# Performance work log

Hardware: AMD Instinct MI355X
Metric: run time of the kernel (lower is better)

Reference implementation:

```python
import jax, jax.numpy as jnp
import numpy as np

N_LAYERS = 2
H = 16                      # num_heads
ARW = (1.0, 1.0)            # att_residual_weight
MCB = (0.0, 1.0)            # mask_clip_balancer
LN_EPS = 1e-5


def _ln(x, g, b):
    mu = jnp.mean(x, axis=-1, keepdims=True)
    var = jnp.mean(jnp.square(x - mu), axis=-1, keepdims=True)
    return (x - mu) * jax.lax.rsqrt(var + LN_EPS) * g + b


def _quick_gelu(u):
    return u * jax.nn.sigmoid(1.702 * u)


def setup_inputs() -> dict:
    key = jax.random.key(0)
    ks = jax.random.split(key, 8)
    L, B, C = 577, 8, 1024
    d_ff = 4 * C
    inp = {
        'x': jax.random.normal(ks[0], (L, B, C), jnp.float32),
        'att_bias': jax.random.normal(ks[1], (N_LAYERS, B * H, L, L), jnp.float32),
        'ln1_g': jnp.ones((N_LAYERS, C), jnp.float32),
        'ln1_b': jnp.zeros((N_LAYERS, C), jnp.float32),
        'in_w': 0.02 * jax.random.normal(ks[2], (N_LAYERS, 3 * C, C), jnp.float32),
        'in_b': jnp.zeros((N_LAYERS, 3 * C), jnp.float32),
        'out_w': 0.02 * jax.random.normal(ks[3], (N_LAYERS, C, C), jnp.float32),
        'out_b': jnp.zeros((N_LAYERS, C), jnp.float32),
        'ln2_g': jnp.ones((N_LAYERS, C), jnp.float32),
        'ln2_b': jnp.zeros((N_LAYERS, C), jnp.float32),
        'fc1_w': 0.02 * jax.random.normal(ks[4], (N_LAYERS, d_ff, C), jnp.float32),
        'fc1_b': jnp.zeros((N_LAYERS, d_ff), jnp.float32),
        'fc2_w': 0.02 * jax.random.normal(ks[5], (N_LAYERS, C, d_ff), jnp.float32),
        'fc2_b': jnp.zeros((N_LAYERS, C), jnp.float32),
    }
    return inp


def reference(x, att_bias, ln1_g, ln1_b, in_w, in_b, out_w, out_b,
              ln2_g, ln2_b, fc1_w, fc1_b, fc2_w, fc2_b):
    L, B, C = x.shape
    d = C // H
    scale = d ** -0.5  # custom_att_factor is None
    for i in range(N_LAYERS):
        # --- custom CSA attention ---
        h = _ln(x, ln1_g[i], ln1_b[i])                              # [L,B,C]
        qkv = jnp.einsum('lbc,fc->lbf', h, in_w[i]) + in_b[i]       # [L,B,3C]
        q, k, v = jnp.split(qkv, 3, axis=-1)
        to_heads = lambda t: t.reshape(L, B, H, d).transpose(1, 2, 0, 3)  # [B,H,L,d]
        q, k, v = to_heads(q), to_heads(k), to_heads(v)
        bias = att_bias[i].reshape(B, H, L, L)
        q_attn = bias + scale * jnp.einsum('bhld,bhmd->bhlm', q, q)
        k_attn = bias + scale * jnp.einsum('bhld,bhmd->bhlm', k, k)
        attn = jax.nn.softmax(q_attn, axis=-1) + jax.nn.softmax(k_attn, axis=-1)
        attn = attn * 0.5                                           # norm_att=True
        attn = jnp.mean(attn, axis=1, keepdims=True)                # avg_att=True -> [B,1,L,L]
        out = jnp.matmul(attn, v)                                   # broadcast over H -> [B,H,L,d]
        out = MCB[0] * v + MCB[1] * out
        out = out.transpose(2, 0, 1, 3).reshape(L, B, C)
        out = jnp.einsum('lbc,oc->lbo', out, out_w[i]) + out_b[i]
        x = ARW[0] * x + ARW[1] * out
        # --- MLP residual ---
        h2 = _ln(x, ln2_g[i], ln2_b[i])
        u = _quick_gelu(jnp.einsum('lbc,fc->lbf', h2, fc1_w[i]) + fc1_b[i])
        x = x + jnp.einsum('lbf,cf->lbc', u, fc2_w[i]) + fc2_b[i]
    return x
```

## Files before the change

### kernel.cpp

```cpp
#include <hip/hip_runtime.h>

typedef float f32x4 __attribute__((ext_vector_type(4)));
typedef __bf16 bf16x8 __attribute__((ext_vector_type(8)));

#define L_SEQ 577
#define BB 8
#define CC 1024
#define HH 16
#define ROWS (L_SEQ*BB)

static __device__ __forceinline__ ushort f2b(float f) {
  unsigned u = __float_as_uint(f);
  u += 0x7fffu + ((u >> 16) & 1u);
  return (ushort)(u >> 16);
}

static __device__ __forceinline__ void gld16(const void* g, void* l) {
  __builtin_amdgcn_global_load_lds((const __attribute__((address_space(1))) void*)g,
                                   (__attribute__((address_space(3))) void*)l, 16, 0, 0);
}

__global__ void cvt_kernel(const float* __restrict__ src, ushort* __restrict__ dst, int n4) {
  int i = blockIdx.x * blockDim.x + threadIdx.x;
  if (i < n4) {
    float4 v = *(const float4*)(src + (size_t)i * 4);
    ushort4 o;
    o.x = f2b(v.x); o.y = f2b(v.y); o.z = f2b(v.z); o.w = f2b(v.w);
    *(ushort4*)(dst + (size_t)i * 4) = o;
  }
}

__global__ __launch_bounds__(256)
void ln_kernel(const float* __restrict__ x, const float* __restrict__ g,
               const float* __restrict__ be, ushort* __restrict__ out)
{
  const int row = blockIdx.x;
  const int t = threadIdx.x;
  const float* xr = x + (size_t)row * CC;
  float4 v = *(const float4*)(xr + t * 4);
  float s  = v.x + v.y + v.z + v.w;
  float s2 = v.x*v.x + v.y*v.y + v.z*v.z + v.w*v.w;
  #pragma unroll
  for (int sd = 1; sd < 64; sd <<= 1) { s += __shfl_xor(s, sd, 64); s2 += __shfl_xor(s2, sd, 64); }
  __shared__ float ps[4], ps2[4];
  const int w = t >> 6;
  if ((t & 63) == 0) { ps[w] = s; ps2[w] = s2; }
  __syncthreads();
  s  = ps[0] + ps[1] + ps[2] + ps[3];
  s2 = ps2[0] + ps2[1] + ps2[2] + ps2[3];
  const float mean = s * (1.f / 1024.f);
  const float var  = s2 * (1.f / 1024.f) - mean * mean;
  const float rstd = rsqrtf(var + 1e-5f);
  float4 gv = *(const float4*)(g + t * 4);
  float4 bv = *(const float4*)(be + t * 4);
  ushort4 o;
  o.x = f2b((v.x - mean) * rstd * gv.x + bv.x);
  o.y = f2b((v.y - mean) * rstd * gv.y + bv.y);
  o.z = f2b((v.z - mean) * rstd * gv.z + bv.z);
  o.w = f2b((v.w - mean) * rstd * gv.w + bv.w);
  *(ushort4*)(out + (size_t)row * CC + t * 4) = o;
}

__global__ __launch_bounds__(256)
void vt_kernel(const ushort* __restrict__ qkv, ushort* __restrict__ vt)
{
  __shared__ ushort tile[32][33];
  const int lt = blockIdx.x * 32;
  const int nt = blockIdx.y * 32;
  const int b  = blockIdx.z;
  const int tx = threadIdx.x & 31;
  const int ty = threadIdx.x >> 5;
  #pragma unroll
  for (int p = 0; p < 4; ++p) {
    int l = lt + ty + p * 8;
    ushort v = 0;
    if (l < L_SEQ) v = qkv[((size_t)l * BB + b) * 3072 + 2048 + nt + tx];
    tile[ty + p * 8][tx] = v;
  }
  __syncthreads();
  #pragma unroll
  for (int p = 0; p < 4; ++p) {
    int n = nt + ty + p * 8;
    int l = lt + tx;
    vt[((size_t)b * 1024 + n) * 608 + l] = tile[tx][ty + p * 8];
  }
}

__global__ __launch_bounds__(256, 2)
void attn_kernel(const ushort* __restrict__ qkv,
                 const float* __restrict__ bias,
                 float* __restrict__ attnf)
{
  __shared__ float S[2][16][612];
  const int t = threadIdx.x;
  const int lane = t & 63;
  const int w = t >> 6;
  const int rb = blockIdx.x;
  const int b  = blockIdx.y;
  const int hg = blockIdx.z;
  const int r0 = rb * 16;
  float acc[37];
  #pragma unroll
  for (int k = 0; k < 37; ++k) acc[k] = 0.f;

  const int fr = lane & 15;
  const int kc = (lane >> 4) * 8;
  const int arow = min(r0 + fr, L_SEQ - 1);
  const size_t abase = ((size_t)arow * BB + b) * 3072;

  for (int hh = 0; hh < 4; ++hh) {
    const int h = hg * 4 + hh;
    const int qoff = h * 64;
    const int koff = CC + h * 64;
    bf16x8 aq0 = *(const bf16x8*)(qkv + abase + qoff + kc);
    bf16x8 aq1 = *(const bf16x8*)(qkv + abase + qoff + 32 + kc);
    bf16x8 ak0 = *(const bf16x8*)(qkv + abase + koff + kc);
    bf16x8 ak1 = *(const bf16x8*)(qkv + abase + koff + 32 + kc);
    for (int nt = w; nt < 37; nt += 4) {
      const int col = nt * 16 + fr;
      const int ncl = min(col, L_SEQ - 1);
      const size_t brow = ((size_t)ncl * BB + b) * 3072;
      bf16x8 bq0 = *(const bf16x8*)(qkv + brow + qoff + kc);
      bf16x8 bq1 = *(const bf16x8*)(qkv + brow + qoff + 32 + kc);
      bf16x8 bk0 = *(const bf16x8*)(qkv + brow + koff + kc);
      bf16x8 bk1 = *(const bf16x8*)(qkv + brow + koff + 32 + kc);
      f32x4 dq = {0.f, 0.f, 0.f, 0.f};
      f32x4 dk = {0.f, 0.f, 0.f, 0.f};
      dq = __builtin_amdgcn_mfma_f32_16x16x32_bf16(aq0, bq0, dq, 0, 0, 0);
      dq = __builtin_amdgcn_mfma_f32_16x16x32_bf16(aq1, bq1, dq, 0, 0, 0);
      dk = __builtin_amdgcn_mfma_f32_16x16x32_bf16(ak0, bk0, dk, 0, 0, 0);
      dk = __builtin_amdgcn_mfma_f32_16x16x32_bf16(ak1, bk1, dk, 0, 0, 0);
      const bool cvalid = (col < L_SEQ);
      #pragma unroll
      for (int r = 0; r < 4; ++r) {
        int row = (lane >> 4) * 4 + r;
        int l = min(r0 + row, L_SEQ - 1);
        float bs = bias[(((size_t)(b * HH + h)) * L_SEQ + l) * L_SEQ + min(col, L_SEQ - 1)];
        S[0][row][col] = cvalid ? (bs + 0.125f * dq[r]) : -1e30f;
        S[1][row][col] = cvalid ? (bs + 0.125f * dk[r]) : -1e30f;
      }
    }
    __syncthreads();
    const int rr = t >> 4;
    const int j0 = t & 15;
    #pragma unroll
    for (int v = 0; v < 2; ++v) {
      float mx = -1e30f;
      #pragma unroll
      for (int k = 0; k < 37; ++k) mx = fmaxf(mx, S[v][rr][j0 + 16 * k]);
      #pragma unroll
      for (int sd = 1; sd < 16; sd <<= 1) mx = fmaxf(mx, __shfl_xor(mx, sd, 16));
      float e[37]; float sm = 0.f;
      #pragma unroll
      for (int k = 0; k < 37; ++k) { e[k] = __expf(S[v][rr][j0 + 16 * k] - mx); sm += e[k]; }
      #pragma unroll
      for (int sd = 1; sd < 16; sd <<= 1) sm += __shfl_xor(sm, sd, 16);
      float inv = 0.03125f / sm;
      #pragma unroll
      for (int k = 0; k < 37; ++k) acc[k] += e[k] * inv;
    }
    __syncthreads();
  }
  const int rr = t >> 4;
  const int j0 = t & 15;
  const int l = r0 + rr;
  if (l < L_SEQ) {
    float* dst = attnf + (size_t)b * 608 * 608 + (size_t)l * 608;
    #pragma unroll
    for (int k = 0; k < 37; ++k)
      if (j0 + 16 * k < L_SEQ) atomicAdd(dst + j0 + 16 * k, acc[k]);
  }
}

template<int EPI>
__global__ __launch_bounds__(256, 2)
void gemm_bt(const ushort* __restrict__ A, int lda, int Arows, long aStride,
             const ushort* __restrict__ B, int ldb, long bStride,
             int M, int N, int K, int kSplit,
             const float* __restrict__ bias,
             float* __restrict__ xio,
             ushort* __restrict__ outb, int ldo)
{
  __shared__ __align__(16) ushort As[128 * 32];
  __shared__ __align__(16) ushort Bs[128 * 32];
  const int t = threadIdx.x;
  const int lane = t & 63;
  const int w = t >> 6;
  const int bm = blockIdx.x, bn = blockIdx.y, bz = blockIdx.z;
  int k0 = 0, k1 = K;
  const ushort* Ab = A;
  const ushort* Bb = B;
  if (kSplit > 1) {
    const int kc0 = K / kSplit;
    k0 = bz * kc0; k1 = k0 + kc0;
  } else {
    Ab += (long)bz * aStride;
    Bb += (long)bz * bStride;
  }
  const int srow = t >> 2;
  const int sc = (t & 3) * 8;
  const int wr = (w >> 1) * 64;
  const int wc = (w & 1) * 64;
  const int am1 = Arows - 1;
  f32x4 acc[4][4] = {};

  const int r0a = bm * 128 + srow;
  const int r0b = bn * 128 + srow;
  for (int kt = k0; kt < k1; kt += 32) {
    __syncthreads();
    gld16(Ab + (size_t)min(r0a, am1) * lda + kt + sc, (void*)(As + t * 8));
    gld16(Ab + (size_t)min(r0a + 64, am1) * lda + kt + sc, (void*)(As + 2048 + t * 8));
    gld16(Bb + (size_t)r0b * ldb + kt + sc, (void*)(Bs + t * 8));
    gld16(Bb + (size_t)(r0b + 64) * ldb + kt + sc, (void*)(Bs + 2048 + t * 8));
    asm volatile("s_waitcnt vmcnt(0)" ::: "memory");
    __syncthreads();
    bf16x8 av[4], bv[4];
    const int fr = lane & 15;
    const int kc = (lane >> 4) * 8;
    #pragma unroll
    for (int m = 0; m < 4; ++m) av[m] = *(const bf16x8*)(As + (wr + m * 16 + fr) * 32 + kc);
    #pragma unroll
    for (int n = 0; n < 4; ++n) bv[n] = *(const bf16x8*)(Bs + (wc + n * 16 + fr) * 32 + kc);
    #pragma unroll
    for (int m = 0; m < 4; ++m)
      #pragma unroll
      for (int n = 0; n < 4; ++n)
        acc[m][n] = __builtin_amdgcn_mfma_f32_16x16x32_bf16(av[m], bv[n], acc[m][n], 0, 0, 0);
  }
  const int rbase = wr + (lane >> 4) * 4;
  const int cbase = wc + (lane & 15);
  #pragma unroll
  for (int n = 0; n < 4; ++n) {
    const int gn = bn * 128 + cbase + n * 16;
    const float bval = (EPI == 3) ? 0.f : ((k0 == 0) ? bias[gn] : 0.f);
    #pragma unroll
    for (int m = 0; m < 4; ++m) {
      f32x4 d = acc[m][n];
      #pragma unroll
      for (int r = 0; r < 4; ++r) {
        const int gm = bm * 128 + rbase + m * 16 + r;
        if (gm < M) {
          if (EPI == 0) {
            outb[(size_t)gm * ldo + gn] = f2b(d[r] + bval);
          } else if (EPI == 1) {
            float v0 = d[r] + bval;
            outb[(size_t)gm * ldo + gn] = f2b(v0 / (1.f + __expf(-1.702f * v0)));
          } else if (EPI == 2) {
            atomicAdd(xio + (size_t)gm * ldo + gn, d[r] + bval);
          } else {
            outb[((size_t)gm * 8 + bz) * ldo + gn] = f2b(d[r]);
          }
        }
      }
    }
  }
}

extern "C" void kernel_launch(void* const* d_in, const int* in_sizes, int n_in,
                              void* d_out, int out_size, void* d_ws, size_t ws_size,
                              hipStream_t stream)
{
  (void)in_sizes; (void)n_in; (void)out_size; (void)ws_size;
  const float* x_in  = (const float*)d_in[0];
  const float* attb  = (const float*)d_in[1];
  const float* ln1_g = (const float*)d_in[2];
  const float* ln1_b = (const float*)d_in[3];
  const float* in_w  = (const float*)d_in[4];
  const float* in_b  = (const float*)d_in[5];
  const float* out_w = (const float*)d_in[6];
  const float* out_b = (const float*)d_in[7];
  const float* ln2_g = (const float*)d_in[8];
  const float* ln2_b = (const float*)d_in[9];
  const float* fc1_w = (const float*)d_in[10];
  const float* fc1_b = (const float*)d_in[11];
  const float* fc2_w = (const float*)d_in[12];
  const float* fc2_b = (const float*)d_in[13];
  float* x = (float*)d_out;

  char* ws = (char*)d_ws;
  size_t off = 0;
  auto alloc = [&](size_t bytes) -> void* {
    void* p = ws + off; off += (bytes + 255) & ~(size_t)255; return p;
  };
  ushort* wIn   = (ushort*)alloc(2ull * 3072 * 1024 * 2);
  ushort* wOut  = (ushort*)alloc(2ull * 1024 * 1024 * 2);
  ushort* wF1   = (ushort*)alloc(2ull * 4096 * 1024 * 2);
  ushort* wF2   = (ushort*)alloc(2ull * 4096 * 1024 * 2);
  ushort* hbuf  = (ushort*)alloc((size_t)ROWS * 1024 * 2);
  ushort* qkv   = (ushort*)alloc((size_t)ROWS * 3072 * 2);
  ushort* vt    = (ushort*)alloc((size_t)8 * 1024 * 608 * 2);
  ushort* attn  = (ushort*)alloc((size_t)8 * 608 * 608 * 2);
  float*  attnf = (float*)alloc((size_t)8 * 608 * 608 * 4);
  ushort* outlb = (ushort*)alloc((size_t)ROWS * 1024 * 2);
  ushort* ubuf  = qkv;

  cvt_kernel<<<2 * 3072 * 1024 / 4 / 256, 256, 0, stream>>>(in_w,  wIn,  2 * 3072 * 1024 / 4);
  cvt_kernel<<<2 * 1024 * 1024 / 4 / 256, 256, 0, stream>>>(out_w, wOut, 2 * 1024 * 1024 / 4);
  cvt_kernel<<<2 * 4096 * 1024 / 4 / 256, 256, 0, stream>>>(fc1_w, wF1,  2 * 4096 * 1024 / 4);
  cvt_kernel<<<2 * 4096 * 1024 / 4 / 256, 256, 0, stream>>>(fc2_w, wF2,  2 * 4096 * 1024 / 4);
  hipMemcpyAsync(x, x_in, (size_t)ROWS * 1024 * 4, hipMemcpyDeviceToDevice, stream);

  for (int i = 0; i < 2; ++i) {
    ln_kernel<<<ROWS, 256, 0, stream>>>(x, ln1_g + i * 1024, ln1_b + i * 1024, hbuf);
    gemm_bt<0><<<dim3(37, 24, 1), 256, 0, stream>>>(hbuf, 1024, ROWS, 0,
        wIn + (size_t)i * 3072 * 1024, 1024, 0,
        ROWS, 3072, 1024, 1, in_b + i * 3072, nullptr, qkv, 3072);
    hipMemsetAsync(attnf, 0, (size_t)8 * 608 * 608 * 4, stream);
    attn_kernel<<<dim3(37, 8, 4), 256, 0, stream>>>(qkv, attb + (size_t)i * 128 * 577 * 577, attnf);
    vt_kernel<<<dim3(19, 32, 8), 256, 0, stream>>>(qkv, vt);
    cvt_kernel<<<8 * 608 * 608 / 4 / 256, 256, 0, stream>>>(attnf, attn, 8 * 608 * 608 / 4);
    gemm_bt<3><<<dim3(5, 8, 8), 256, 0, stream>>>(attn, 608, 577, (long)608 * 608,
        vt, 608, (long)1024 * 608,
        577, 1024, 608, 1, nullptr, nullptr, outlb, 1024);
    gemm_bt<2><<<dim3(37, 8, 2), 256, 0, stream>>>(outlb, 1024, ROWS, 0,
        wOut + (size_t)i * 1024 * 1024, 1024, 0,
        ROWS, 1024, 1024, 2, out_b + i * 1024, x, nullptr, 1024);
    ln_kernel<<<ROWS, 256, 0, stream>>>(x, ln2_g + i * 1024, ln2_b + i * 1024, hbuf);
    gemm_bt<1><<<dim3(37, 32, 1), 256, 0, stream>>>(hbuf, 1024, ROWS, 0,
        wF1 + (size_t)i * 4096 * 1024, 1024, 0,
        ROWS, 4096, 1024, 1, fc1_b + i * 4096, nullptr, ubuf, 4096);
    gemm_bt<2><<<dim3(37, 8, 4), 256, 0, stream>>>(ubuf, 4096, ROWS, 0,
        wF2 + (size_t)i * 4096 * 1024, 4096, 0,
        ROWS, 1024, 4096, 4, fc2_b + i * 1024, x, nullptr, 1024);
  }
}
```

Before: 1.146 ms.

## Add 256x256 pipelined GEMM with split-K partials reduced in fused LN-residual kernel

Replaces the 128x128 single-buffered GEMM for the QKV, out-proj, FC1 and FC2 projections with a 512-thread 256x256 tile kernel. The new kernel double-buffers 64-wide K tiles in a swizzled LDS layout and interleaves MFMA quadrants with async global-to-LDS loads, using barriers and setprio. Split-K outputs are no longer atomically added into x. They are written as fp32 partials and summed, together with the bias and residual, inside a new kernel that also computes the next LayerNorm, which removes the separate LN launches and the initial memcpy. The cost is 128KB of LDS per block at occupancy 1, fewer blocks (tile quantization on 4616 rows), and extra partial-buffer traffic.

New measurement: 1.912 ms. +66.9%, slower.

```diff
diff --git a/kernel.cpp b/kernel.cpp
--- a/kernel.cpp
+++ b/kernel.cpp
@@ -30,35 +30,49 @@
   }
 }
 
+template<int NP, bool DOLN>
 __global__ __launch_bounds__(256)
-void ln_kernel(const float* __restrict__ x, const float* __restrict__ g,
-               const float* __restrict__ be, ushort* __restrict__ out)
+void ln_resid_kernel(const float* __restrict__ xsrc, const float* __restrict__ parts,
+                     const float* __restrict__ cbias,
+                     const float* __restrict__ g, const float* __restrict__ be,
+                     float* __restrict__ xdst, ushort* __restrict__ hout)
 {
   const int row = blockIdx.x;
   const int t = threadIdx.x;
-  const float* xr = x + (size_t)row * CC;
-  float4 v = *(const float4*)(xr + t * 4);
-  float s  = v.x + v.y + v.z + v.w;
-  float s2 = v.x*v.x + v.y*v.y + v.z*v.z + v.w*v.w;
-  #pragma unroll
-  for (int sd = 1; sd < 64; sd <<= 1) { s += __shfl_xor(s, sd, 64); s2 += __shfl_xor(s2, sd, 64); }
-  __shared__ float ps[4], ps2[4];
-  const int w = t >> 6;
-  if ((t & 63) == 0) { ps[w] = s; ps2[w] = s2; }
-  __syncthreads();
-  s  = ps[0] + ps[1] + ps[2] + ps[3];
-  s2 = ps2[0] + ps2[1] + ps2[2] + ps2[3];
-  const float mean = s * (1.f / 1024.f);
-  const float var  = s2 * (1.f / 1024.f) - mean * mean;
-  const float rstd = rsqrtf(var + 1e-5f);
-  float4 gv = *(const float4*)(g + t * 4);
-  float4 bv = *(const float4*)(be + t * 4);
-  ushort4 o;
-  o.x = f2b((v.x - mean) * rstd * gv.x + bv.x);
-  o.y = f2b((v.y - mean) * rstd * gv.y + bv.y);
-  o.z = f2b((v.z - mean) * rstd * gv.z + bv.z);
-  o.w = f2b((v.w - mean) * rstd * gv.w + bv.w);
-  *(ushort4*)(out + (size_t)row * CC + t * 4) = o;
+  float4 v = *(const float4*)(xsrc + (size_t)row * CC + t * 4);
+  if (NP > 0) {
+    float4 c4 = *(const float4*)(cbias + t * 4);
+    v.x += c4.x; v.y += c4.y; v.z += c4.z; v.w += c4.w;
+    #pragma unroll
+    for (int p = 0; p < NP; ++p) {
+      float4 pv = *(const float4*)(parts + ((size_t)p * ROWS + row) * CC + t * 4);
+      v.x += pv.x; v.y += pv.y; v.z += pv.z; v.w += pv.w;
+    }
+  }
+  *(float4*)(xdst + (size_t)row * CC + t * 4) = v;
+  if (DOLN) {
+    float s  = v.x + v.y + v.z + v.w;
+    float s2 = v.x*v.x + v.y*v.y + v.z*v.z + v.w*v.w;
+    #pragma unroll
+    for (int sd = 1; sd < 64; sd <<= 1) { s += __shfl_xor(s, sd, 64); s2 += __shfl_xor(s2, sd, 64); }
+    __shared__ float ps[4], ps2[4];
+    const int w = t >> 6;
+    if ((t & 63) == 0) { ps[w] = s; ps2[w] = s2; }
+    __syncthreads();
+    s  = ps[0] + ps[1] + ps[2] + ps[3];
+    s2 = ps2[0] + ps2[1] + ps2[2] + ps2[3];
+    const float mean = s * (1.f / 1024.f);
+    const float var  = s2 * (1.f / 1024.f) - mean * mean;
+    const float rstd = rsqrtf(var + 1e-5f);
+    float4 gv = *(const float4*)(g + t * 4);
+    float4 bv = *(const float4*)(be + t * 4);
+    ushort4 o;
+    o.x = f2b((v.x - mean) * rstd * gv.x + bv.x);
+    o.y = f2b((v.y - mean) * rstd * gv.y + bv.y);
+    o.z = f2b((v.z - mean) * rstd * gv.z + bv.z);
+    o.w = f2b((v.w - mean) * rstd * gv.w + bv.w);
+    *(ushort4*)(hout + (size_t)row * CC + t * 4) = o;
+  }
 }
 
 __global__ __launch_bounds__(256)
@@ -172,13 +186,10 @@
   }
 }
 
-template<int EPI>
 __global__ __launch_bounds__(256, 2)
-void gemm_bt(const ushort* __restrict__ A, int lda, int Arows, long aStride,
+void av_gemm(const ushort* __restrict__ A, int lda, int Arows, long aStride,
              const ushort* __restrict__ B, int ldb, long bStride,
-             int M, int N, int K, int kSplit,
-             const float* __restrict__ bias,
-             float* __restrict__ xio,
+             int M, int K,
              ushort* __restrict__ outb, int ldo)
 {
   __shared__ __align__(16) ushort As[128 * 32];
@@ -187,16 +198,8 @@
   const int lane = t & 63;
   const int w = t >> 6;
   const int bm = blockIdx.x, bn = blockIdx.y, bz = blockIdx.z;
-  int k0 = 0, k1 = K;
-  const ushort* Ab = A;
-  const ushort* Bb = B;
-  if (kSplit > 1) {
-    const int kc0 = K / kSplit;
-    k0 = bz * kc0; k1 = k0 + kc0;
-  } else {
-    Ab += (long)bz * aStride;
-    Bb += (long)bz * bStride;
-  }
+  const ushort* Ab = A + (long)bz * aStride;
+  const ushort* Bb = B + (long)bz * bStride;
   const int srow = t >> 2;
   const int sc = (t & 3) * 8;
   const int wr = (w >> 1) * 64;
@@ -206,7 +209,7 @@
 
   const int r0a = bm * 128 + srow;
   const int r0b = bn * 128 + srow;
-  for (int kt = k0; kt < k1; kt += 32) {
+  for (int kt = 0; kt < K; kt += 32) {
     __syncthreads();
     gld16(Ab + (size_t)min(r0a, am1) * lda + kt + sc, (void*)(As + t * 8));
     gld16(Ab + (size_t)min(r0a + 64, am1) * lda + kt + sc, (void*)(As + 2048 + t * 8));
@@ -232,23 +235,149 @@
   #pragma unroll
   for (int n = 0; n < 4; ++n) {
     const int gn = bn * 128 + cbase + n * 16;
-    const float bval = (EPI == 3) ? 0.f : ((k0 == 0) ? bias[gn] : 0.f);
     #pragma unroll
     for (int m = 0; m < 4; ++m) {
       f32x4 d = acc[m][n];
       #pragma unroll
       for (int r = 0; r < 4; ++r) {
         const int gm = bm * 128 + rbase + m * 16 + r;
+        if (gm < M) outb[((size_t)gm * 8 + bz) * ldo + gn] = f2b(d[r]);
+      }
+    }
+  }
+}
+
+#define MFQ(MH, NH) \
+  _Pragma("unroll") \
+  for (int ks = 0; ks < 2; ++ks) \
+    _Pragma("unroll") \
+    for (int m = 0; m < 4; ++m) \
+      _Pragma("unroll") \
+      for (int n = 0; n < 2; ++n) \
+        acc[(MH)*4+m][(NH)*2+n] = __builtin_amdgcn_mfma_f32_16x16x32_bf16( \
+            (MH) ? Ahi[ks][m] : Alo[ks][m], (NH) ? Bhi[ks][n] : Blo[ks][n], \
+            acc[(MH)*4+m][(NH)*2+n], 0, 0, 0);
+
+#define KTILE(BOFS, KT2, MORE, DRAIN) do { \
+  _Pragma("unroll") for (int ks = 0; ks < 2; ++ks) { \
+    _Pragma("unroll") for (int m = 0; m < 4; ++m) Alo[ks][m] = rdA(BOFS, 0, ks, m); \
+    _Pragma("unroll") for (int n = 0; n < 2; ++n) Blo[ks][n] = rdB(BOFS, 0, ks, n); \
+  } \
+  asm volatile("s_waitcnt lgkmcnt(8)" ::: "memory"); \
+  __builtin_amdgcn_sched_barrier(0); \
+  __builtin_amdgcn_s_barrier(); \
+  asm volatile("s_waitcnt lgkmcnt(0)" ::: "memory"); \
+  __builtin_amdgcn_sched_barrier(0); \
+  __builtin_amdgcn_s_setprio(1); MFQ(0,0) __builtin_amdgcn_s_setprio(0); \
+  __builtin_amdgcn_s_barrier(); \
+  _Pragma("unroll") for (int ks = 0; ks < 2; ++ks) { \
+    _Pragma("unroll") for (int m = 0; m < 4; ++m) Ahi[ks][m] = rdA(BOFS, 1, ks, m); \
+    _Pragma("unroll") for (int n = 0; n < 2; ++n) Bhi[ks][n] = rdB(BOFS, 1, ks, n); \
+  } \
+  asm volatile("s_waitcnt lgkmcnt(8)" ::: "memory"); \
+  __builtin_amdgcn_sched_barrier(0); \
+  __builtin_amdgcn_s_barrier(); \
+  asm volatile("s_waitcnt lgkmcnt(0)" ::: "memory"); \
+  __builtin_amdgcn_sched_barrier(0); \
+  __builtin_amdgcn_s_setprio(1); MFQ(1,1) __builtin_amdgcn_s_setprio(0); \
+  __builtin_amdgcn_s_barrier(); \
+  if (MORE) { stageA(KT2, BOFS, 0); stageA(KT2, BOFS, 1); } \
+  __builtin_amdgcn_s_barrier(); \
+  __builtin_amdgcn_s_setprio(1); MFQ(0,1) __builtin_amdgcn_s_setprio(0); \
+  __builtin_amdgcn_s_barrier(); \
+  if (MORE) { stageB(KT2, BOFS, 0); stageB(KT2, BOFS, 1); } \
+  __builtin_amdgcn_s_barrier(); \
+  __builtin_amdgcn_s_setprio(1); MFQ(1,0) __builtin_amdgcn_s_setprio(0); \
+  if (MORE)       asm volatile("s_waitcnt vmcnt(6)" ::: "memory"); \
+  else if (DRAIN) asm volatile("s_waitcnt vmcnt(0)" ::: "memory"); \
+  __builtin_amdgcn_sched_barrier(0); \
+  __builtin_amdgcn_s_barrier(); \
+} while (0)
+
+template<int EPI>
+__global__ __launch_bounds__(512, 1)
+void gemm8(const ushort* __restrict__ Ap, int lda, int Arows,
+           const ushort* __restrict__ Bp, int ldb,
+           int M, int Ksplit,
+           const float* __restrict__ bias,
+           ushort* __restrict__ outb, float* __restrict__ outf, int ldo)
+{
+  __shared__ __align__(16) char smem[131072];
+  const int t = threadIdx.x;
+  const int lane = t & 63;
+  const int w = t >> 6;
+  const int wm = w >> 2, wn = w & 3;
+  const int bm = blockIdx.x, bn = blockIdx.y, bz = blockIdx.z;
+  const int k0 = bz * Ksplit;
+  const int nkt = Ksplit >> 6;
+  const int iters = nkt >> 1;
+  const int am1 = Arows - 1;
+  const int fr = lane & 15;
+  const int lq = lane >> 4;
+
+  f32x4 acc[8][4] = {};
+  bf16x8 Alo[2][4], Ahi[2][4], Blo[2][2], Bhi[2][2];
+
+  auto stageA = [&](int kt, int bofs, int half) {
+    #pragma unroll
+    for (int j = 0; j < 2; ++j) {
+      const int idx = t + j * 512;
+      const int row = idx >> 3, cb = idx & 7;
+      const int gr = min(bm * 256 + half * 128 + row, am1);
+      gld16(Ap + (size_t)gr * lda + k0 + kt * 64 + ((cb ^ (row & 7)) << 3),
+            smem + bofs + half * 16384 + idx * 16);
+    }
+  };
+  auto stageB = [&](int kt, int bofs, int half) {
+    #pragma unroll
+    for (int j = 0; j < 2; ++j) {
+      const int idx = t + j * 512;
+      const int row = idx >> 3, cb = idx & 7;
+      const int gr = bn * 256 + half * 128 + row;
+      gld16(Bp + (size_t)gr * ldb + k0 + kt * 64 + ((cb ^ (row & 7)) << 3),
+            smem + bofs + 32768 + half * 16384 + idx * 16);
+    }
+  };
+  auto rdA = [&](int bofs, int mh, int ks, int m) -> bf16x8 {
+    const int row = wm * 128 + mh * 64 + m * 16 + fr;
+    const int cb  = (ks * 4 + lq) ^ (fr & 7);
+    return *(const bf16x8*)(smem + bofs + row * 128 + cb * 16);
+  };
+  auto rdB = [&](int bofs, int nh, int ks, int n) -> bf16x8 {
+    const int row = wn * 64 + nh * 32 + n * 16 + fr;
+    const int cb  = (ks * 4 + lq) ^ (fr & 7);
+    return *(const bf16x8*)(smem + bofs + 32768 + row * 128 + cb * 16);
+  };
+
+  stageA(0, 0, 0); stageA(0, 0, 1); stageB(0, 0, 0); stageB(0, 0, 1);
+  stageA(1, 65536, 0); stageA(1, 65536, 1); stageB(1, 65536, 0); stageB(1, 65536, 1);
+  asm volatile("s_waitcnt vmcnt(8)" ::: "memory");
+  __builtin_amdgcn_sched_barrier(0);
+  __builtin_amdgcn_s_barrier();
+
+  for (int i = 0; i < iters; ++i) {
+    const bool more = (i + 1 < iters);
+    KTILE(0,     2 * i + 2, more, true);
+    KTILE(65536, 2 * i + 3, more, false);
+  }
+
+  #pragma unroll
+  for (int g = 0; g < 8; ++g) {
+    #pragma unroll
+    for (int n = 0; n < 4; ++n) {
+      const int gn = bn * 256 + wn * 64 + n * 16 + fr;
+      f32x4 d = acc[g][n];
+      #pragma unroll
+      for (int r = 0; r < 4; ++r) {
+        const int gm = bm * 256 + wm * 128 + g * 16 + lq * 4 + r;
         if (gm < M) {
           if (EPI == 0) {
-            outb[(size_t)gm * ldo + gn] = f2b(d[r] + bval);
+            outb[(size_t)gm * ldo + gn] = f2b(d[r] + bias[gn]);
           } else if (EPI == 1) {
-            float v0 = d[r] + bval;
+            float v0 = d[r] + bias[gn];
             outb[(size_t)gm * ldo + gn] = f2b(v0 / (1.f + __expf(-1.702f * v0)));
-          } else if (EPI == 2) {
-            atomicAdd(xio + (size_t)gm * ldo + gn, d[r] + bval);
           } else {
-            outb[((size_t)gm * 8 + bz) * ldo + gn] = f2b(d[r]);
+            outf[((size_t)bz * M + gm) * ldo + gn] = d[r];
           }
         }
       }
@@ -292,35 +421,43 @@
   ushort* attn  = (ushort*)alloc((size_t)8 * 608 * 608 * 2);
   float*  attnf = (float*)alloc((size_t)8 * 608 * 608 * 4);
   ushort* outlb = (ushort*)alloc((size_t)ROWS * 1024 * 2);
+  float*  pbuf  = (float*)alloc((size_t)4 * ROWS * 1024 * 4);
   ushort* ubuf  = qkv;
 
   cvt_kernel<<<2 * 3072 * 1024 / 4 / 256, 256, 0, stream>>>(in_w,  wIn,  2 * 3072 * 1024 / 4);
   cvt_kernel<<<2 * 1024 * 1024 / 4 / 256, 256, 0, stream>>>(out_w, wOut, 2 * 1024 * 1024 / 4);
   cvt_kernel<<<2 * 4096 * 1024 / 4 / 256, 256, 0, stream>>>(fc1_w, wF1,  2 * 4096 * 1024 / 4);
   cvt_kernel<<<2 * 4096 * 1024 / 4 / 256, 256, 0, stream>>>(fc2_w, wF2,  2 * 4096 * 1024 / 4);
-  hipMemcpyAsync(x, x_in, (size_t)ROWS * 1024 * 4, hipMemcpyDeviceToDevice, stream);
+  ln_resid_kernel<0, true><<<ROWS, 256, 0, stream>>>(x_in, nullptr, nullptr,
+      ln1_g, ln1_b, x, hbuf);
 
   for (int i = 0; i < 2; ++i) {
-    ln_kernel<<<ROWS, 256, 0, stream>>>(x, ln1_g + i * 1024, ln1_b + i * 1024, hbuf);
-    gemm_bt<0><<<dim3(37, 24, 1), 256, 0, stream>>>(hbuf, 1024, ROWS, 0,
-        wIn + (size_t)i * 3072 * 1024, 1024, 0,
-        ROWS, 3072, 1024, 1, in_b + i * 3072, nullptr, qkv, 3072);
+    gemm8<0><<<dim3(19, 12, 1), 512, 0, stream>>>(hbuf, 1024, ROWS,
+        wIn + (size_t)i * 3072 * 1024, 1024,
+        ROWS, 1024, in_b + i * 3072, qkv, nullptr, 3072);
     hipMemsetAsync(attnf, 0, (size_t)8 * 608 * 608 * 4, stream);
     attn_kernel<<<dim3(37, 8, 4), 256, 0, stream>>>(qkv, attb + (size_t)i * 128 * 577 * 577, attnf);
     vt_kernel<<<dim3(19, 32, 8), 256, 0, stream>>>(qkv, vt);
     cvt_kernel<<<8 * 608 * 608 / 4 / 256, 256, 0, stream>>>(attnf, attn, 8 * 608 * 608 / 4);
-    gemm_bt<3><<<dim3(5, 8, 8), 256, 0, stream>>>(attn, 608, 577, (long)608 * 608,
-        vt, 608, (long)1024 * 608,
-        577, 1024, 608, 1, nullptr, nullptr, outlb, 1024);
-    gemm_bt<2><<<dim3(37, 8, 2), 256, 0, stream>>>(outlb, 1024, ROWS, 0,
-        wOut + (size_t)i * 1024 * 1024, 1024, 0,
-        ROWS, 1024, 1024, 2, out_b + i * 1024, x, nullptr, 1024);
-    ln_kernel<<<ROWS, 256, 0, stream>>>(x, ln2_g + i * 1024, ln2_b + i * 1024, hbuf);
-    gemm_bt<1><<<dim3(37, 32, 1), 256, 0, stream>>>(hbuf, 1024, ROWS, 0,
-        wF1 + (size_t)i * 4096 * 1024, 1024, 0,
-        ROWS, 4096, 1024, 1, fc1_b + i * 4096, nullptr, ubuf, 4096);
-    gemm_bt<2><<<dim3(37, 8, 4), 256, 0, stream>>>(ubuf, 4096, ROWS, 0,
-        wF2 + (size_t)i * 4096 * 1024, 4096, 0,
-        ROWS, 1024, 4096, 4, fc2_b + i * 1024, x, nullptr, 1024);
-  }
-}
+    av_gemm<<<dim3(5, 8, 8), 256, 0, stream>>>(attn, 608, 577, (long)608 * 608,
+        vt, 608, (long)1024 * 608, 577, 608, outlb, 1024);
+    gemm8<4><<<dim3(19, 4, 2), 512, 0, stream>>>(outlb, 1024, ROWS,
+        wOut + (size_t)i * 1024 * 1024, 1024,
+        ROWS, 512, nullptr, nullptr, pbuf, 1024);
+    ln_resid_kernel<2, true><<<ROWS, 256, 0, stream>>>(x, pbuf, out_b + i * 1024,
+        ln2_g + i * 1024, ln2_b + i * 1024, x, hbuf);
+    gemm8<1><<<dim3(19, 16, 1), 512, 0, stream>>>(hbuf, 1024, ROWS,
+        wF1 + (size_t)i * 4096 * 1024, 1024,
+        ROWS, 1024, fc1_b + i * 4096, ubuf, nullptr, 4096);
+    gemm8<4><<<dim3(19, 4, 4), 512, 0, stream>>>(ubuf, 4096, ROWS,
+        wF2 + (size_t)i * 4096 * 1024, 4096,
+        ROWS, 1024, nullptr, nullptr, pbuf, 1024);
+    if (i == 0) {
+      ln_resid_kernel<4, true><<<ROWS, 256, 0, stream>>>(x, pbuf, fc2_b,
+          ln1_g + 1024, ln1_b + 1024, x, hbuf);
+    } else {
+      ln_resid_kernel<4, false><<<ROWS, 256, 0, stream>>>(x, pbuf, fc2_b + 1024,
+          nullptr, nullptr, x, nullptr);
+    }
+  }
+}
```
